# Performance work log

Measured on AMD Instinct MI355X. Metric: run time of the kernel, lower is better.

Reference implementation:

```python
import jax, jax.numpy as jnp
import numpy as np

B, L, D, H = 32, 256, 2048, 8
DH = D // H  # 256; code requires L == S == DH


def setup_inputs() -> dict:
    key = jax.random.key(0)
    ks = jax.random.split(key, 12)
    s = 1.0 / np.sqrt(D)
    return {
        "queries": jax.random.normal(ks[0], (B, L, D), jnp.float32),
        "keys": jax.random.normal(ks[1], (B, L, D), jnp.float32),
        "values": jax.random.normal(ks[2], (B, L, D), jnp.float32),
        "Wq": jax.random.normal(ks[3], (D, D), jnp.float32) * s,
        "bq": jax.random.normal(ks[4], (D,), jnp.float32) * s,
        "Wk": jax.random.normal(ks[5], (D, D), jnp.float32) * s,
        "bk": jax.random.normal(ks[6], (D,), jnp.float32) * s,
        "Wv": jax.random.normal(ks[7], (D, D), jnp.float32) * s,
        "bv": jax.random.normal(ks[8], (D,), jnp.float32) * s,
        "Wo": jax.random.normal(ks[9], (D, D), jnp.float32) * s,
        "bo": jax.random.normal(ks[10], (D,), jnp.float32) * s,
        "temperature": jnp.ones((H, 1, 1), jnp.float32),
    }


def reference(queries, keys, values, Wq, bq, Wk, bk, Wv, bv, Wo, bo, temperature):
    b, l, d = queries.shape
    # projections (Linear: x @ W^T + b)
    q = (jnp.einsum('bld,ed->ble', queries, Wq) + bq).reshape(b, l, H, DH).transpose(0, 2, 1, 3)   # [B,H,L,dh]
    k = (jnp.einsum('bsd,ed->bse', keys, Wk) + bk).reshape(b, l, H, DH).transpose(0, 2, 1, 3)      # [B,H,S,dh]
    v = (jnp.einsum('bsd,ed->bse', values, Wv) + bv).reshape(b, l, H, DH).transpose(0, 2, 3, 1)    # [B,H,dh,S]
    # FFT cross-correlation over the head dim (as in the source)
    qf = jnp.fft.rfft(q, axis=-1)
    kf = jnp.fft.rfft(k, axis=-1)
    corr = jnp.fft.irfft(qf * jnp.conj(kf), n=DH, axis=-1)   # [B,H,L,dh]
    corr = jax.nn.softmax(corr / temperature, axis=-1)
    # dropout is identity in eval mode
    # time-delay aggregation: [B,H,dh,S] @ [B,H,dh,L] (S == dh) -> [B,H,dh,L]
    out = jnp.matmul(v, jnp.swapaxes(corr, -1, -2))
    out = out.transpose(0, 3, 1, 2).reshape(b, l, d)          # [B,L,D]
    out = jnp.einsum('bld,ed->ble', out, Wo) + bo
    return out
```

## Files before the change

kernel.cpp:

```cpp
#include <hip/hip_runtime.h>
#include <stdint.h>

typedef float  f32x4 __attribute__((ext_vector_type(4)));
typedef short  s16x8 __attribute__((ext_vector_type(8)));
typedef _Float16 h16x8 __attribute__((ext_vector_type(8)));
typedef _Float16 h16x2 __attribute__((ext_vector_type(2)));
typedef unsigned short u16x4 __attribute__((ext_vector_type(4)));
typedef unsigned int u32x2 __attribute__((ext_vector_type(2)));
typedef unsigned int u32x4 __attribute__((ext_vector_type(4)));

#define DEV __device__ __forceinline__

DEV unsigned short f2bf(float f) {
  union { float f; unsigned int u; } v; v.f = f;
  unsigned int u = v.u;
  return (unsigned short)((u + 0x7fffu + ((u >> 16) & 1u)) >> 16);
}

typedef const __attribute__((address_space(1))) void* as1cvp;
typedef __attribute__((address_space(3))) void* as3vp;
DEV void gload16(const void* g, void* l) {
  __builtin_amdgcn_global_load_lds((as1cvp)g, (as3vp)l, 16, 0, 0);
}

DEV float fdot2u(unsigned int a, unsigned int b, float c) {
  return __builtin_amdgcn_fdot2(__builtin_bit_cast(h16x2, a),
                                __builtin_bit_cast(h16x2, b), c, false);
}


template<int M0, int M1, int M2>
__global__ __launch_bounds__(256)
void pack3(const float* __restrict__ in0, unsigned short* __restrict__ out0, long n0,
           const float* __restrict__ in1, unsigned short* __restrict__ out1, long n1,
           const float* __restrict__ in2, unsigned short* __restrict__ out2, long n2)
{
  const long total = n0 + n1 + n2;
  for (long t = (long)blockIdx.x * 256 + threadIdx.x; t < total;
       t += (long)gridDim.x * 256) {
    const float* src; unsigned short* dst; long i; int mode;
    if (t < n0)           { src = in0; dst = out0; i = t;           mode = M0; }
    else if (t < n0 + n1) { src = in1; dst = out1; i = t - n0;      mode = M1; }
    else                  { src = in2; dst = out2; i = t - n0 - n1; mode = M2; }
    f32x4 x0 = *(const f32x4*)(src + i * 8);
    f32x4 x1 = *(const f32x4*)(src + i * 8 + 4);
    s16x8 h8;
    #pragma unroll
    for (int e = 0; e < 4; ++e) {
      if (mode == 1) {
        h8[e]     = (short)__builtin_bit_cast(unsigned short, (_Float16)x0[e]);
        h8[e + 4] = (short)__builtin_bit_cast(unsigned short, (_Float16)x1[e]);
      } else {
        h8[e]     = (short)f2bf(x0[e]);
        h8[e + 4] = (short)f2bf(x1[e]);
      }
    }
    *(s16x8*)(dst + i * 8) = h8;
  }
}

template<int M0, int M1, int M2, int M3>
__global__ __launch_bounds__(256)
void pack4(const float* __restrict__ in0, unsigned short* __restrict__ out0, long n0,
           const float* __restrict__ in1, unsigned short* __restrict__ out1, long n1,
           const float* __restrict__ in2, unsigned short* __restrict__ out2, long n2,
           const float* __restrict__ in3, unsigned short* __restrict__ out3, long n3)
{
  const long total = n0 + n1 + n2 + n3;
  for (long t = (long)blockIdx.x * 256 + threadIdx.x; t < total;
       t += (long)gridDim.x * 256) {
    const float* src; unsigned short* dst; long i; int mode;
    if (t < n0)                { src = in0; dst = out0; i = t;                mode = M0; }
    else if (t < n0 + n1)      { src = in1; dst = out1; i = t - n0;           mode = M1; }
    else if (t < n0 + n1 + n2) { src = in2; dst = out2; i = t - n0 - n1;      mode = M2; }
    else                       { src = in3; dst = out3; i = t - n0 - n1 - n2; mode = M3; }
    f32x4 x0 = *(const f32x4*)(src + i * 8);
    f32x4 x1 = *(const f32x4*)(src + i * 8 + 4);
    s16x8 h8;
    #pragma unroll
    for (int e = 0; e < 4; ++e) {
      if (mode == 1) {
        h8[e]     = (short)__builtin_bit_cast(unsigned short, (_Float16)x0[e]);
        h8[e + 4] = (short)__builtin_bit_cast(unsigned short, (_Float16)x1[e]);
      } else {
        h8[e]     = (short)f2bf(x0[e]);
        h8[e + 4] = (short)f2bf(x1[e]);
      }
    }
    *(s16x8*)(dst + i * 8) = h8;
  }
}


#define GEMM8P_CORE(DT, APTR, BPTR, M0EXPR, N0EXPR)                           \
  constexpr int LD  = 2048;                                                   \
  constexpr int NT  = 32;                                                     \
  constexpr int NI  = NT / 2;                                                 \
  __shared__ __align__(16) unsigned short lds[65536];                         \
  const int tid  = threadIdx.x;                                               \
  const int lane = tid & 63;                                                  \
  const int wid  = tid >> 6;                                                  \
  const int wm   = wid >> 2;                                                  \
  const int wn   = wid & 3;                                                   \
  const int fr   = lane & 15;                                                 \
  const int ko   = (lane >> 4) * 8;                                           \
  const int m0 = (M0EXPR) * 256;                                              \
  const int n0 = (N0EXPR) * 256;                                              \
  const int sr  = tid >> 3;                                                   \
  const int scc = (((tid & 7) ^ (((tid >> 5) & 1) << 2)) << 3);               \
  auto sA = [&](int d, int u, int col) {                                      \
    const unsigned short* s0 = (APTR) + (long)(m0 + u * 64 + sr) * LD + col + scc; \
    const int lb = d * 32768 + u * 4096 + (wid << 9);                         \
    gload16(s0, lds + lb);                                                    \
    gload16(s0 + 128 * LD, lds + lb + 8192);                                  \
  };                                                                          \
  auto sB = [&](int d, int h2, int col) {                                     \
    const unsigned short* s0 = (BPTR) + (long)(n0 + h2 * 128 + sr) * LD + col + scc; \
    const int lb = d * 32768 + 16384 + h2 * 8192 + (wid << 9);                \
    gload16(s0, lds + lb);                                                    \
    gload16(s0 + 64 * LD, lds + lb + 4096);                                   \
  };                                                                          \
  f32x4 acc[8][4];                                                            \
  _Pragma("unroll") for (int i = 0; i < 8; ++i)                               \
    _Pragma("unroll") for (int j = 0; j < 4; ++j)                             \
      acc[i][j] = (f32x4)(0.0f);                                              \
  s16x8 afr[2][2], bfr[4][2];                                                 \
  sB(0, 0, 0); sB(0, 1, 0);                                                   \
  sA(0, 0, 0); sA(0, 1, 0);                                                   \
  sB(1, 0, 64); sB(1, 1, 64);                                                 \
  sA(1, 0, 64);                                                               \
  asm volatile("s_waitcnt vmcnt(6)" ::: "memory");                            \
  __builtin_amdgcn_s_barrier();                                               \
  for (int i = 0; i < NI; ++i) {                                              \
    const int a1c = (2 * i + 1) << 6;                                         \
    const int c0  = ((2 * i + 2 < NT) ? 2 * i + 2 : NT - 1) << 6;             \
    const int c1  = ((2 * i + 3 < NT) ? 2 * i + 3 : NT - 1) << 6;             \
    PHASE(DT, 0, 0, true,  sA(1, 1, a1c), false)                              \
    PHASE(DT, 0, 1, false, sB(0, 0, c0), false)                               \
    PHASE(DT, 0, 2, false, sB(0, 1, c0), false)                               \
    PHASE(DT, 0, 3, false, sA(0, 0, c0), true)                                \
    PHASE(DT, 1, 0, true,  sA(0, 1, c0), false)                               \
    PHASE(DT, 1, 1, false, sB(1, 0, c1), false)                               \
    PHASE(DT, 1, 2, false, sB(1, 1, c1), false)                               \
    PHASE(DT, 1, 3, false, sA(1, 0, c1), true)                                \
  }

template<int DT>
DEV f32x4 mfma16(s16x8 a, s16x8 b, f32x4 c) {
  if constexpr (DT == 0)
    return __builtin_amdgcn_mfma_f32_16x16x32_bf16(a, b, c, 0, 0, 0);
  else
    return __builtin_amdgcn_mfma_f32_16x16x32_f16(
        __builtin_bit_cast(h16x8, a), __builtin_bit_cast(h16x8, b), c, 0, 0, 0);
}

#define LOADB(d)                                                              \
  _Pragma("unroll") for (int ni = 0; ni < 4; ++ni)                            \
    _Pragma("unroll") for (int kk = 0; kk < 2; ++kk) {                        \
      const int nr = wn * 64 + ni * 16 + fr;                                  \
      int u = (d) * 32768 + 16384 + (nr >> 7) * 8192 + (nr & 127) * 64        \
              + kk * 32 + ko;                                                 \
      u ^= ((u >> 8) & 1) << 5;                                               \
      bfr[ni][kk] = *(const s16x8*)&lds[u];                                   \
    }

#define PHASE(DT, d, q, DOB, STAGE, VM)                                       \
  {                                                                           \
    if (DOB) { LOADB(d) }                                                     \
    _Pragma("unroll") for (int ai = 0; ai < 2; ++ai)                          \
      _Pragma("unroll") for (int kk = 0; kk < 2; ++kk) {                      \
        int u = (d) * 32768 + wm * 8192 + ((2 * (q) + ai) * 16 + fr) * 64     \
                + kk * 32 + ko;                                               \
        u ^= ((u >> 8) & 1) << 5;                                             \
        afr[ai][kk] = *(const s16x8*)&lds[u];                                 \
      }                                                                       \
    STAGE;                                                                    \
    __builtin_amdgcn_s_barrier();                                             \
    asm volatile("s_waitcnt lgkmcnt(0)" ::: "memory");                        \
    __builtin_amdgcn_sched_barrier(0);                                        \
    __builtin_amdgcn_s_setprio(1);                                            \
    _Pragma("unroll") for (int ai = 0; ai < 2; ++ai)                          \
      _Pragma("unroll") for (int ni = 0; ni < 4; ++ni)                        \
        _Pragma("unroll") for (int kk = 0; kk < 2; ++kk)                      \
          acc[2 * (q) + ai][ni] =                                             \
              mfma16<DT>(afr[ai][kk], bfr[ni][kk], acc[2 * (q) + ai][ni]);    \
    __builtin_amdgcn_s_setprio(0);                                            \
    if (VM) { asm volatile("s_waitcnt vmcnt(6)" ::: "memory"); }              \
    __builtin_amdgcn_s_barrier();                                             \
  }

template<int DT, int OM>
__global__ __launch_bounds__(512, 2)
void gemm8p(const unsigned short* __restrict__ Ap, const unsigned short* __restrict__ Bp,
            const float* __restrict__ bias, void* __restrict__ Cp)
{
  const int bx = blockIdx.x;
  GEMM8P_CORE(DT, Ap, Bp, ((bx & 7) << 2) + (bx >> 3), blockIdx.y)

  const int rg = (lane >> 4) * 4;
  #pragma unroll
  for (int ni = 0; ni < 4; ++ni) {
    const int gn = n0 + wn * 64 + ni * 16 + fr;
    const float bvl = bias[gn];
    #pragma unroll
    for (int mi = 0; mi < 8; ++mi) {
      const int gmB = m0 + wm * 128 + mi * 16 + rg;
      f32x4 v = acc[mi][ni];
      if (OM == 0) {
        float* Cf = (float*)Cp;
        #pragma unroll
        for (int r = 0; r < 4; ++r)
          Cf[(long)(gmB + r) * 2048 + gn] = v[r] + bvl;
      } else {
        unsigned short* Ch = (unsigned short*)Cp;
        #pragma unroll
        for (int r = 0; r < 4; ++r)
          Ch[(long)(gmB + r) * 2048 + gn] =
              __builtin_bit_cast(unsigned short, (_Float16)(v[r] + bvl));
      }
    }
  }
}

__global__ __launch_bounds__(512, 2)
void qkv8p(const unsigned short* __restrict__ Ap,
           const unsigned short* __restrict__ Bq, const unsigned short* __restrict__ Bk,
           const unsigned short* __restrict__ Bv,
           const float* __restrict__ bq, const float* __restrict__ bk,
           const float* __restrict__ bv,
           unsigned short* __restrict__ Cq, unsigned short* __restrict__ Ck,
           unsigned short* __restrict__ Cv)
{
  const int bid = blockIdx.x;
  const int idx = bid >> 3;
  const int pre_m0 = (bid & 7) * 12 + (idx >> 3);
  const int seg = pre_m0 >> 5;
  const unsigned short* Bp = (seg == 0) ? Bq : (seg == 1) ? Bk : Bv;
  const float* bias = (seg == 0) ? bq : (seg == 1) ? bk : bv;

  GEMM8P_CORE(1, Ap, Bp, pre_m0, idx & 7)

  const int rg = (lane >> 4) * 4;
  const int m0l = m0 & 8191;
  if (seg < 2) {
    unsigned short* Ch = (seg == 0) ? Cq : Ck;
    #pragma unroll
    for (int ni = 0; ni < 4; ++ni) {
      const int gn = n0 + wn * 64 + ni * 16 + fr;
      const float bvl = bias[gn];
      #pragma unroll
      for (int mi = 0; mi < 8; ++mi) {
        const int gmB = m0l + wm * 128 + mi * 16 + rg;
        f32x4 v = acc[mi][ni];
        #pragma unroll
        for (int r = 0; r < 4; ++r)
          Ch[(long)(gmB + r) * 2048 + gn] =
              __builtin_bit_cast(unsigned short, (_Float16)(v[r] + bvl));
      }
    }
  } else {
    #pragma unroll
    for (int ni = 0; ni < 4; ++ni) {
      const int gn = n0 + wn * 64 + ni * 16 + fr;
      const float bvl = bias[gn];
      #pragma unroll
      for (int mi = 0; mi < 8; ++mi) {
        const int gmB = m0l + wm * 128 + mi * 16 + rg;
        f32x4 v = acc[mi][ni];
        const int b = gmB >> 8, s = gmB & 255, h = gn >> 8, ii = gn & 255;
        u16x4 o;
        #pragma unroll
        for (int r = 0; r < 4; ++r) o[r] = f2bf(v[r] + bvl);
        *(u16x4*)&Cv[((long)((b * 8 + h) * 256 + ii) << 8) + s] = o;
      }
    }
  }
}

__global__ __launch_bounds__(256)
void fgemm_agg(const unsigned short* __restrict__ A, const unsigned short* __restrict__ B,
               void* __restrict__ C)
{
  constexpr int lda = 256, ldb = 256, ldc = 2048, KT = 256;
  __shared__ __align__(16) unsigned short lA[2 * 128 * 32];
  __shared__ __align__(16) unsigned short lB[2 * 128 * 32];

  const int tid  = threadIdx.x;
  const int lane = tid & 63;
  const int wid  = tid >> 6;
  const int wr   = wid >> 1;
  const int wc   = wid & 1;

  const int z  = blockIdx.z;
  const int m0 = blockIdx.y * 128;
  const int n0 = blockIdx.x * 128;

  long aBase = (long)m0 * lda + (long)z * 256 * lda;
  long bBase = (long)n0 * ldb + (long)z * 256 * ldb;

  const int ar0 = tid >> 2, ac0 = (tid & 3) * 8;
  const int ar1 = ar0 + 64;

  const unsigned short* pa0 = A + aBase + (long)ar0 * lda + ac0;
  const unsigned short* pa1 = A + aBase + (long)ar1 * lda + ac0;
  const unsigned short* pb0 = B + bBase + (long)ar0 * ldb + ac0;
  const unsigned short* pb1 = B + bBase + (long)ar1 * ldb + ac0;

  f32x4 acc[4][4];
  #pragma unroll
  for (int i = 0; i < 4; ++i)
    #pragma unroll
    for (int j = 0; j < 4; ++j)
      acc[i][j] = (f32x4)(0.0f);

  const int fr   = lane & 15;
  const int krow = (lane >> 4) * 8;

  for (int kt = 0; kt < KT; kt += 64) {
    gload16(pa0 + kt,      lA + tid * 8);
    gload16(pa1 + kt,      lA + (tid + 256) * 8);
    gload16(pa0 + kt + 32, lA + 4096 + tid * 8);
    gload16(pa1 + kt + 32, lA + 4096 + (tid + 256) * 8);
    gload16(pb0 + kt,      lB + tid * 8);
    gload16(pb1 + kt,      lB + (tid + 256) * 8);
    gload16(pb0 + kt + 32, lB + 4096 + tid * 8);
    gload16(pb1 + kt + 32, lB + 4096 + (tid + 256) * 8);
    __syncthreads();

    s16x8 a0[4], a1[4], b0[4], b1[4];
    #pragma unroll
    for (int i = 0; i < 4; ++i) {
      const int r = (wr * 64 + i * 16 + fr) * 32 + krow;
      a0[i] = *(const s16x8*)&lA[r];
      a1[i] = *(const s16x8*)&lA[4096 + r];
    }
    #pragma unroll
    for (int j = 0; j < 4; ++j) {
      const int r = (wc * 64 + j * 16 + fr) * 32 + krow;
      b0[j] = *(const s16x8*)&lB[r];
      b1[j] = *(const s16x8*)&lB[4096 + r];
    }

    #pragma unroll
    for (int i = 0; i < 4; ++i)
      #pragma unroll
      for (int j = 0; j < 4; ++j) {
        acc[i][j] = __builtin_amdgcn_mfma_f32_16x16x32_bf16(a0[i], b0[j], acc[i][j], 0, 0, 0);
        acc[i][j] = __builtin_amdgcn_mfma_f32_16x16x32_bf16(a1[i], b1[j], acc[i][j], 0, 0, 0);
      }

    __syncthreads();
  }

  const int rg = (lane >> 4) * 4;
  #pragma unroll
  for (int j = 0; j < 4; ++j) {
    const int gn = n0 + wc * 64 + j * 16 + fr;
    #pragma unroll
    for (int i = 0; i < 4; ++i) {
      const int gmB = m0 + wr * 64 + i * 16 + rg;
      f32x4 v = acc[i][j];
      long cb = (long)(z >> 3) * 256 * ldc + (long)(z & 7) * 256;
      unsigned short* Ch = (unsigned short*)C;
      #pragma unroll
      for (int r = 0; r < 4; ++r)
        Ch[cb + (long)(gmB + r) * ldc + gn] = f2bf(v[r]);
    }
  }
}

__global__ __launch_bounds__(256)
void corr_softmax(const unsigned short* __restrict__ qp,
                  const unsigned short* __restrict__ kp,
                  const float* __restrict__ temp, unsigned short* __restrict__ w)
{
  __shared__ __align__(16) unsigned short qs[4][520];
  __shared__ __align__(16) unsigned short q2[4][520];
  __shared__ __align__(16) unsigned short ks[4][264];
  const int tid  = threadIdx.x;
  const int lane = tid & 63;
  const int wid  = tid >> 6;
  const int row  = blockIdx.x * 4 + wid;
  const int b = row >> 11;
  const int h = (row >> 8) & 7;
  const int l = row & 255;
  const long base = ((long)(b * 256 + l) << 11) + h * 256;

  {
    u16x4 qv = *(const u16x4*)(qp + base + 4 * lane);
    u16x4 kv = *(const u16x4*)(kp + base + 4 * lane);
    const int nxt = __shfl((int)(unsigned int)(unsigned short)qv[0],
                           (lane + 1) & 63, 64);
    u16x4 qsv;
    qsv[0] = qv[1]; qsv[1] = qv[2]; qsv[2] = qv[3];
    qsv[3] = (unsigned short)(unsigned int)nxt;
    *(u16x4*)&qs[wid][4 * lane]       = qv;
    *(u16x4*)&qs[wid][256 + 4 * lane] = qv;
    *(u16x4*)&q2[wid][4 * lane]       = qsv;
    *(u16x4*)&q2[wid][256 + 4 * lane] = qsv;
    *(u16x4*)&ks[wid][4 * lane]       = kv;
  }
  __syncthreads();

  const unsigned short* Q  = &qs[wid][0];
  const unsigned short* Qs = &q2[wid][0];
  const unsigned short* K  = &ks[wid][0];
  const int e = 2 * lane;

  u32x2 A  = *(const u32x2*)&Q[2 * e];
  u32x2 B  = *(const u32x2*)&Q[2 * (e + 2)];
  u32x2 C  = *(const u32x2*)&Q[2 * (e + 4)];
  u32x2 A2 = *(const u32x2*)&Qs[2 * e];
  u32x2 B2 = *(const u32x2*)&Qs[2 * (e + 2)];
  u32x2 C2 = *(const u32x2*)&Qs[2 * (e + 4)];

  float c0 = 0.f, c1 = 0.f, c2 = 0.f, c3 = 0.f;

  #pragma unroll 2
  for (int t = 0; t < 32; ++t) {
    u32x4 Kw = *(const u32x4*)&K[8 * t];
    const unsigned int p0 = A[0],  p1 = A[1],  p2 = B[0],  p3 = B[1],  p4 = C[0];
    const unsigned int s0 = A2[0], s1 = A2[1], s2 = B2[0], s3 = B2[1], s4 = C2[0];
    c0 = fdot2u(Kw[0], p0, c0); c2 = fdot2u(Kw[0], p1, c2);
    c1 = fdot2u(Kw[0], s0, c1); c3 = fdot2u(Kw[0], s1, c3);
    c0 = fdot2u(Kw[1], p1, c0); c2 = fdot2u(Kw[1], p2, c2);
    c1 = fdot2u(Kw[1], s1, c1); c3 = fdot2u(Kw[1], s2, c3);
    c0 = fdot2u(Kw[2], p2, c0); c2 = fdot2u(Kw[2], p3, c2);
    c1 = fdot2u(Kw[2], s2, c1); c3 = fdot2u(Kw[2], s3, c3);
    c0 = fdot2u(Kw[3], p3, c0); c2 = fdot2u(Kw[3], p4, c2);
    c1 = fdot2u(Kw[3], s3, c1); c3 = fdot2u(Kw[3], s4, c3);
    A = C;  A2 = C2;
    B  = *(const u32x2*)&Q[2 * (4 * t + e + 6)];
    C  = *(const u32x2*)&Q[2 * (4 * t + e + 8)];
    B2 = *(const u32x2*)&Qs[2 * (4 * t + e + 6)];
    C2 = *(const u32x2*)&Qs[2 * (4 * t + e + 8)];
  }

  const float invT = 1.0f / temp[h];
  float mx = fmaxf(fmaxf(c0, c1), fmaxf(c2, c3));
  #pragma unroll
  for (int off = 32; off >= 1; off >>= 1) mx = fmaxf(mx, __shfl_xor(mx, off, 64));
  const float e0 = __expf((c0 - mx) * invT);
  const float e1 = __expf((c1 - mx) * invT);
  const float e2 = __expf((c2 - mx) * invT);
  const float e3 = __expf((c3 - mx) * invT);
  float sm = e0 + e1 + e2 + e3;
  #pragma unroll
  for (int off = 32; off >= 1; off >>= 1) sm += __shfl_xor(sm, off, 64);
  const float rs = 1.0f / sm;
  u16x4 o;
  o[0] = f2bf(e0 * rs); o[1] = f2bf(e1 * rs); o[2] = f2bf(e2 * rs); o[3] = f2bf(e3 * rs);
  *(u16x4*)(w + (long)row * 256 + 4 * lane) = o;
}


extern "C" void kernel_launch(void* const* d_in, const int* in_sizes, int n_in,
                              void* d_out, int out_size, void* d_ws, size_t ws_size,
                              hipStream_t stream) {
  (void)in_sizes; (void)n_in; (void)out_size; (void)ws_size;
  const float* queries = (const float*)d_in[0];
  const float* keys    = (const float*)d_in[1];
  const float* values  = (const float*)d_in[2];
  const float* Wq = (const float*)d_in[3];
  const float* bq = (const float*)d_in[4];
  const float* Wk = (const float*)d_in[5];
  const float* bk = (const float*)d_in[6];
  const float* Wv = (const float*)d_in[7];
  const float* bv = (const float*)d_in[8];
  const float* Wo = (const float*)d_in[9];
  const float* bo = (const float*)d_in[10];
  const float* temp = (const float*)d_in[11];

  char* ws = (char*)d_ws;
  auto MB = [](size_t m) { return m << 20; };
  unsigned short* qA   = (unsigned short*)ws;
  unsigned short* wgt  = (unsigned short*)ws;
  unsigned short* kA   = (unsigned short*)(ws + MB(32));
  unsigned short* out2 = (unsigned short*)(ws + MB(32));
  unsigned short* vA   = (unsigned short*)(ws + MB(64));
  unsigned short* qproj= (unsigned short*)(ws + MB(96));
  unsigned short* kproj= (unsigned short*)(ws + MB(128));
  unsigned short* WqF  = (unsigned short*)(ws + MB(160));
  unsigned short* WkF  = (unsigned short*)(ws + MB(168));
  unsigned short* WvF  = (unsigned short*)(ws + MB(176));
  unsigned short* WoB  = (unsigned short*)(ws + MB(184));
  unsigned short* vT   = (unsigned short*)d_out;

  dim3 blk(256);
  const long nBig = (long)8192 * 2048 / 8;
  const long nW   = (long)2048 * 2048 / 8;

  pack4<1, 1, 1, 1><<<2048, blk, 0, stream>>>(queries, qA, nBig, keys, kA, nBig,
                                              values, vA, nBig, Wq, WqF, nW);
  pack3<1, 1, 0><<<2048, blk, 0, stream>>>(Wk, WkF, nW, Wv, WvF, nW, Wo, WoB, nW);
  qkv8p<<<dim3(768), 512, 0, stream>>>(qA, WqF, WkF, WvF, bq, bk, bv,
                                       qproj, kproj, vT);
  corr_softmax<<<dim3(16384), blk, 0, stream>>>(qproj, kproj, temp, wgt);
  fgemm_agg<<<dim3(2, 2, 256), blk, 0, stream>>>(wgt, vT, out2);
  gemm8p<0, 0><<<dim3(32, 8), 512, 0, stream>>>(out2, WoB, bo, (float*)d_out);
}
```

Measured before the change: 463.2 us.

## Split fused QKV projection into three separate GEMM launches

Replaces the single 768-block qkv8p kernel, which computed the Q, K and V projections in one launch, with three launches of the generic gemm8p template. A new output mode handles the transposed bf16 V store. The V projection is moved after corr_softmax. This trades one large launch for smaller ones and extra launch overhead, possibly to get a simpler schedule or better L2 behaviour. It may also make the wave tail worse because each launch has only 256 blocks.

```diff
diff --git a/kernel.cpp b/kernel.cpp
--- a/kernel.cpp
+++ b/kernel.cpp
@@ -211,67 +211,18 @@
         #pragma unroll
         for (int r = 0; r < 4; ++r)
           Cf[(long)(gmB + r) * 2048 + gn] = v[r] + bvl;
-      } else {
+      } else if (OM == 2) {
         unsigned short* Ch = (unsigned short*)Cp;
         #pragma unroll
         for (int r = 0; r < 4; ++r)
           Ch[(long)(gmB + r) * 2048 + gn] =
               __builtin_bit_cast(unsigned short, (_Float16)(v[r] + bvl));
-      }
-    }
-  }
-}
-
-__global__ __launch_bounds__(512, 2)
-void qkv8p(const unsigned short* __restrict__ Ap,
-           const unsigned short* __restrict__ Bq, const unsigned short* __restrict__ Bk,
-           const unsigned short* __restrict__ Bv,
-           const float* __restrict__ bq, const float* __restrict__ bk,
-           const float* __restrict__ bv,
-           unsigned short* __restrict__ Cq, unsigned short* __restrict__ Ck,
-           unsigned short* __restrict__ Cv)
-{
-  const int bid = blockIdx.x;
-  const int idx = bid >> 3;
-  const int pre_m0 = (bid & 7) * 12 + (idx >> 3);
-  const int seg = pre_m0 >> 5;
-  const unsigned short* Bp = (seg == 0) ? Bq : (seg == 1) ? Bk : Bv;
-  const float* bias = (seg == 0) ? bq : (seg == 1) ? bk : bv;
-
-  GEMM8P_CORE(1, Ap, Bp, pre_m0, idx & 7)
-
-  const int rg = (lane >> 4) * 4;
-  const int m0l = m0 & 8191;
-  if (seg < 2) {
-    unsigned short* Ch = (seg == 0) ? Cq : Ck;
-    #pragma unroll
-    for (int ni = 0; ni < 4; ++ni) {
-      const int gn = n0 + wn * 64 + ni * 16 + fr;
-      const float bvl = bias[gn];
-      #pragma unroll
-      for (int mi = 0; mi < 8; ++mi) {
-        const int gmB = m0l + wm * 128 + mi * 16 + rg;
-        f32x4 v = acc[mi][ni];
-        #pragma unroll
-        for (int r = 0; r < 4; ++r)
-          Ch[(long)(gmB + r) * 2048 + gn] =
-              __builtin_bit_cast(unsigned short, (_Float16)(v[r] + bvl));
-      }
-    }
-  } else {
-    #pragma unroll
-    for (int ni = 0; ni < 4; ++ni) {
-      const int gn = n0 + wn * 64 + ni * 16 + fr;
-      const float bvl = bias[gn];
-      #pragma unroll
-      for (int mi = 0; mi < 8; ++mi) {
-        const int gmB = m0l + wm * 128 + mi * 16 + rg;
-        f32x4 v = acc[mi][ni];
+      } else {
         const int b = gmB >> 8, s = gmB & 255, h = gn >> 8, ii = gn & 255;
         u16x4 o;
         #pragma unroll
         for (int r = 0; r < 4; ++r) o[r] = f2bf(v[r] + bvl);
-        *(u16x4*)&Cv[((long)((b * 8 + h) * 256 + ii) << 8) + s] = o;
+        *(u16x4*)&((unsigned short*)Cp)[((long)((b * 8 + h) * 256 + ii) << 8) + s] = o;
       }
     }
   }
@@ -487,15 +438,17 @@
   unsigned short* vT   = (unsigned short*)d_out;
 
   dim3 blk(256);
+  dim3 gBig(32, 8);
   const long nBig = (long)8192 * 2048 / 8;
   const long nW   = (long)2048 * 2048 / 8;
 
   pack4<1, 1, 1, 1><<<2048, blk, 0, stream>>>(queries, qA, nBig, keys, kA, nBig,
                                               values, vA, nBig, Wq, WqF, nW);
   pack3<1, 1, 0><<<2048, blk, 0, stream>>>(Wk, WkF, nW, Wv, WvF, nW, Wo, WoB, nW);
-  qkv8p<<<dim3(768), 512, 0, stream>>>(qA, WqF, WkF, WvF, bq, bk, bv,
-                                       qproj, kproj, vT);
+  gemm8p<1, 2><<<gBig, 512, 0, stream>>>(qA, WqF, bq, qproj);
+  gemm8p<1, 2><<<gBig, 512, 0, stream>>>(kA, WkF, bk, kproj);
   corr_softmax<<<dim3(16384), blk, 0, stream>>>(qproj, kproj, temp, wgt);
+  gemm8p<1, 1><<<gBig, 512, 0, stream>>>(vA, WvF, bv, vT);
   fgemm_agg<<<dim3(2, 2, 256), blk, 0, stream>>>(wgt, vT, out2);
-  gemm8p<0, 0><<<dim3(32, 8), 512, 0, stream>>>(out2, WoB, bo, (float*)d_out);
-}
+  gemm8p<0, 0><<<gBig, 512, 0, stream>>>(out2, WoB, bo, (float*)d_out);
+}
```

Result: no change. 459.9 us (-0.7%).
